# Performance work log

Measured on AMD Instinct MI355X. Metric: run time of the kernel, lower is better.

## Reference

```python
import jax, jax.numpy as jnp
import numpy as np

D = 1e-6
B, N, E, K = 128, 512, 512, 256


def _lower_median_abs(x, axis):
    # torch.median returns the LOWER of the two middle values for even counts
    n = x.shape[axis]
    s = jnp.sort(jnp.abs(x), axis=axis)
    return jnp.take(s, (n - 1) // 2, axis=axis)


def _bounds_from_cauchy(head, errors, k):
    # errors: (B, E, *head.shape[1:]); E divisible by k in this config
    b, e = errors.shape[0], errors.shape[1]
    tail = errors.shape[2:]
    chunks = errors.reshape(b, e // k, k, *tail)
    l1 = _lower_median_abs(chunks, axis=2).sum(axis=1)
    return head - l1, head + l1


def _relaxed_exp(h, errs, noise, lb, ub):
    is_tight = ub == lb
    lam_s = (jnp.exp(ub) - jnp.exp(lb)) / (ub - lb + D)
    lam = jnp.minimum(lam_s, jnp.exp(lb + 1.0 - 0.1))
    ub0 = jnp.where(lam > lam_s, jnp.exp(lb) - lam * lb, jnp.exp(ub) - lam * ub)
    mu = 0.5 * (lam * (1.0 - jnp.log(lam)) + ub0)
    delta = 0.5 * (ub0 - lam * (1.0 - jnp.log(lam)))
    lam = jnp.where(is_tight, 0.0, lam)
    mu = jnp.where(is_tight, jnp.exp(ub), mu)
    delta = jnp.where(is_tight, 0.0, delta)
    new_head = h * lam + mu
    new_errs = jnp.concatenate([errs * lam[:, None], delta[:, None] * noise], axis=1)
    return new_head, new_errs


def _relaxed_log(h, errs, noise, lb, ub):
    is_tight = ub == lb
    lam_s = (jnp.log(ub) - jnp.log(lb + D)) / (ub - lb + D)
    lam = lam_s
    lb0 = jnp.where(lam < lam_s, jnp.log(ub) - ub * lam, jnp.log(lb + D) - lb * lam)
    mu = 0.5 * (-jnp.log(lam) - 1.0 + lb0)
    delta = 0.5 * (-jnp.log(lam) - 1.0 - lb0)
    lam = jnp.where(is_tight, 0.0, lam)
    mu = jnp.where(is_tight, jnp.log(ub), mu)
    delta = jnp.where(is_tight, 0.0, delta)
    new_head = h * lam + mu
    new_errs = jnp.concatenate([errs * lam[:, None], delta[:, None] * noise], axis=1)
    return new_head, new_errs


def setup_inputs() -> dict:
    key = jax.random.key(0)
    k1, k2, k3, k4 = jax.random.split(key, 4)
    curr_head = jax.random.normal(k1, (B, N), dtype=jnp.float32)
    # small error magnitudes keep exp/log relaxation bounds valid (lb of log stage > 0)
    curr_errors = 1e-3 * jax.random.normal(k2, (B * E, N), dtype=jnp.float32)
    cauchy_exp = jax.random.cauchy(k3, (B, K, N), dtype=jnp.float32)
    cauchy_log = jax.random.cauchy(k4, (B, K), dtype=jnp.float32)
    return {"curr_head": curr_head, "curr_errors": curr_errors,
            "cauchy_exp": cauchy_exp, "cauchy_log": cauchy_log, "k": K}


def reference(curr_head, curr_errors, cauchy_exp, cauchy_log, k):
    b, n = curr_head.shape
    max_head = jax.lax.stop_gradient(jnp.max(curr_head, axis=1, keepdims=True))  # (B,1)
    temp_head = curr_head - max_head                         # (B,N)
    errs = curr_errors.reshape(b, -1, n)                     # (B,E,N)
    lb, ub = _bounds_from_cauchy(temp_head, errs, k)
    exp_head, exp_errs = _relaxed_exp(temp_head, errs, cauchy_exp, lb, ub)  # (B,N),(B,E+K,N)
    exp_head = exp_head.sum(axis=1)                          # (B,)
    exp_errs = exp_errs.sum(axis=2)                          # (B,E+K)
    lb2, ub2 = _bounds_from_cauchy(exp_head, exp_errs, k)
    ls_head, ls_errs = _relaxed_log(exp_head, exp_errs, cauchy_log, lb2, ub2)  # (B,),(B,E+2K)
    ls_head = ls_head + max_head[:, 0]
    return ls_head, ls_errs.reshape(-1)
```

## Files before the change

### kernel.cpp

```cpp
#include <hip/hip_runtime.h>
#include <cstdint>
#include <cstddef>

#define BB 128
#define NN 512
#define EE 512
#define KK 256
#define STR 17

__device__ __forceinline__ float wave_reduce_max(float v) {
#pragma unroll
  for (int off = 32; off >= 1; off >>= 1) v = fmaxf(v, __shfl_xor(v, off, 64));
  return v;
}
__device__ __forceinline__ float wave_reduce_sum(float v) {
#pragma unroll
  for (int off = 32; off >= 1; off >>= 1) v += __shfl_xor(v, off, 64);
  return v;
}

template <int CTRL>
__device__ __forceinline__ float dppz(float x) {
  return __int_as_float(__builtin_amdgcn_update_dpp(0, __float_as_int(x), CTRL, 0xf, 0xf, false));
}
template <int CTRL>
__device__ __forceinline__ float dppi(float x) {
  return __int_as_float(__builtin_amdgcn_update_dpp(__float_as_int(x), __float_as_int(x), CTRL, 0xf, 0xf, false));
}
__device__ __forceinline__ float wave_sum64(float x) {
  x += dppz<0x111>(x); x += dppz<0x112>(x); x += dppz<0x114>(x); x += dppz<0x118>(x);
  x += dppz<0x142>(x); x += dppz<0x143>(x);
  return __int_as_float(__builtin_amdgcn_readlane(__float_as_int(x), 63));
}
__device__ __forceinline__ float wave_max64nn(float x) {
  x = fmaxf(x, dppz<0x111>(x)); x = fmaxf(x, dppz<0x112>(x));
  x = fmaxf(x, dppz<0x114>(x)); x = fmaxf(x, dppz<0x118>(x));
  x = fmaxf(x, dppz<0x142>(x)); x = fmaxf(x, dppz<0x143>(x));
  return __int_as_float(__builtin_amdgcn_readlane(__float_as_int(x), 63));
}
__device__ __forceinline__ float wave_min64(float x) {
  x = fminf(x, dppi<0x111>(x)); x = fminf(x, dppi<0x112>(x));
  x = fminf(x, dppi<0x114>(x)); x = fminf(x, dppi<0x118>(x));
  x = fminf(x, dppi<0x142>(x)); x = fminf(x, dppi<0x143>(x));
  return __int_as_float(__builtin_amdgcn_readlane(__float_as_int(x), 63));
}

__device__ __forceinline__ float wave_median256_fast(float a0, float a1, float a2, float a3) {
  float S = wave_sum64((a0 + a1) + (a2 + a3));
  float mean = S * 0.00390625f;
  float lo = 0.f, hi = S * 1.0000002f + 1e-37f;
  int c_lo = 0, c_hi = 256;
  float piv = 0.845f * mean;
  float ans = 0.f;
  bool have = false;
#pragma unroll 1
  for (int it = 0; it < 34; ++it) {
    if (!(piv > lo && piv < hi)) piv = 0.5f * (lo + hi);
    int cnt = __popcll(__ballot(a0 < piv)) + __popcll(__ballot(a1 < piv)) +
              __popcll(__ballot(a2 < piv)) + __popcll(__ballot(a3 < piv));
    if (cnt == 128) {
      float m = fmaxf(fmaxf(a0 < piv ? a0 : 0.f, a1 < piv ? a1 : 0.f),
                      fmaxf(a2 < piv ? a2 : 0.f, a3 < piv ? a3 : 0.f));
      ans = wave_max64nn(m); have = true; break;
    }
    if (cnt == 127) {
      float m = fminf(fminf(a0 >= piv ? a0 : 3.4e38f, a1 >= piv ? a1 : 3.4e38f),
                      fminf(a2 >= piv ? a2 : 3.4e38f, a3 >= piv ? a3 : 3.4e38f));
      ans = wave_min64(m); have = true; break;
    }
    if (cnt < 127) { lo = piv; c_lo = cnt; } else { hi = piv; c_hi = cnt; }
    if (it == 0) piv = piv + (127.5f - (float)cnt) * mean * 0.0077f;
    else piv = lo + (hi - lo) * ((127.5f - (float)c_lo) / (float)(c_hi - c_lo));
    if (it >= 10) piv = 0.5f * (lo + hi);
  }
  if (!have) {
    float m = fmaxf(fmaxf(a0 < hi ? a0 : 0.f, a1 < hi ? a1 : 0.f),
                    fmaxf(a2 < hi ? a2 : 0.f, a3 < hi ? a3 : 0.f));
    ans = wave_max64nn(m);
  }
  return ans;
}

__global__ __launch_bounds__(1024, 8) void kfused(
    const float* __restrict__ head, const float* __restrict__ errs,
    float* __restrict__ ws_delta, float* __restrict__ ws_htpart,
    float* __restrict__ ws_epart) {
  __shared__ float tile[512 * STR];
  __shared__ float medbuf[32];
  __shared__ float lambuf[16];
  __shared__ float redm[16];
  const int blk = blockIdx.x;
  const int b = blk >> 5, g = blk & 31;
  const int n0 = g * 16;
  const int tid = threadIdx.x, wave = tid >> 6, lane = tid & 63;

  float m = (tid < NN) ? head[(size_t)b * NN + tid] : -3.4e38f;
  m = wave_reduce_max(m);
  if (lane == 0) redm[wave] = m;

  const int tr = tid >> 2, tc = (tid & 3) * 4;
  const float* src = errs + (size_t)b * EE * NN + n0 + tc;
#pragma unroll
  for (int i = 0; i < 2; ++i) {
    int row = i * 256 + tr;
    float4 v = *(const float4*)(src + (size_t)row * NN);
    float* dst = &tile[row * STR + tc];
    dst[0] = v.x; dst[1] = v.y; dst[2] = v.z; dst[3] = v.w;
  }
  __syncthreads();

#pragma unroll 1
  for (int j = 0; j < 2; ++j) {
    int p = wave * 2 + j;
    int col = p & 15;
    int rb = (p >> 4) * 256;
    float a0 = fabsf(tile[(rb + lane) * STR + col]);
    float a1 = fabsf(tile[(rb + lane + 64) * STR + col]);
    float a2 = fabsf(tile[(rb + lane + 128) * STR + col]);
    float a3 = fabsf(tile[(rb + lane + 192) * STR + col]);
    float med = wave_median256_fast(a0, a1, a2, a3);
    if (lane == 0) medbuf[p] = med;
  }
  __syncthreads();

  float htp = 0.f;
  if (tid < 16) {
    float hmax = fmaxf(
        fmaxf(fmaxf(fmaxf(redm[0], redm[1]), fmaxf(redm[2], redm[3])),
              fmaxf(fmaxf(redm[4], redm[5]), fmaxf(redm[6], redm[7]))),
        fmaxf(fmaxf(fmaxf(redm[8], redm[9]), fmaxf(redm[10], redm[11])),
              fmaxf(fmaxf(redm[12], redm[13]), fmaxf(redm[14], redm[15]))));
    int n = n0 + tid;
    float l1 = medbuf[tid] + medbuf[16 + tid];
    float th = head[(size_t)b * NN + n] - hmax;
    float lb = th - l1, ub = th + l1;
    float lam, mu, delta;
    if (ub == lb) {
      lam = 0.f; mu = expf(ub); delta = 0.f;
    } else {
      float elb = expf(lb), eub = expf(ub);
      float lam_s = (eub - elb) / (ub - lb + 1e-6f);
      lam = fminf(lam_s, expf(lb + 0.9f));
      float ub0 = (lam > lam_s) ? (elb - lam * lb) : (eub - lam * ub);
      float t = lam * (1.f - logf(lam));
      mu = 0.5f * (t + ub0);
      delta = 0.5f * (ub0 - t);
    }
    lambuf[tid] = lam;
    ws_delta[(size_t)b * NN + n] = delta;
    htp = th * lam + mu;
  }
  if (wave == 0) {
    float s = wave_reduce_sum(htp);
    if (lane == 0) ws_htpart[b * 32 + g] = s;
  }
  __syncthreads();

  if (tid < NN) {
    float s0 = 0.f;
#pragma unroll
    for (int j = 0; j < 16; ++j) s0 = fmaf(tile[tid * STR + j], lambuf[j], s0);
    ws_epart[((size_t)(b * 32 + g)) * 512 + tid] = s0;
  }
}

__global__ __launch_bounds__(256) void kcexp(
    const float* __restrict__ cexp, const float* __restrict__ ws_delta,
    float* __restrict__ ws_ee2) {
  const int blk = blockIdx.x;
  const int b = blk >> 4, seg = blk & 15;
  const int wave = threadIdx.x >> 6, lane = threadIdx.x & 63;
  const float* wsrc = ws_delta + (size_t)b * NN;
  float4 wa = *(const float4*)(wsrc + 4 * lane);
  float4 wb = *(const float4*)(wsrc + 256 + 4 * lane);
  const int r0 = seg * 16 + wave * 4;
  const float* base = cexp + (size_t)b * KK * NN;
  float* out = ws_ee2 + (size_t)b * KK;
  float s0, s1, s2, s3;
  {
    const float* rp = base + (size_t)r0 * NN;
    float4 x = *(const float4*)(rp + 4 * lane);
    float4 y = *(const float4*)(rp + 256 + 4 * lane);
    s0 = x.x * wa.x + x.y * wa.y + x.z * wa.z + x.w * wa.w +
         y.x * wb.x + y.y * wb.y + y.z * wb.z + y.w * wb.w;
  }
  {
    const float* rp = base + (size_t)(r0 + 1) * NN;
    float4 x = *(const float4*)(rp + 4 * lane);
    float4 y = *(const float4*)(rp + 256 + 4 * lane);
    s1 = x.x * wa.x + x.y * wa.y + x.z * wa.z + x.w * wa.w +
         y.x * wb.x + y.y * wb.y + y.z * wb.z + y.w * wb.w;
  }
  {
    const float* rp = base + (size_t)(r0 + 2) * NN;
    float4 x = *(const float4*)(rp + 4 * lane);
    float4 y = *(const float4*)(rp + 256 + 4 * lane);
    s2 = x.x * wa.x + x.y * wa.y + x.z * wa.z + x.w * wa.w +
         y.x * wb.x + y.y * wb.y + y.z * wb.z + y.w * wb.w;
  }
  {
    const float* rp = base + (size_t)(r0 + 3) * NN;
    float4 x = *(const float4*)(rp + 4 * lane);
    float4 y = *(const float4*)(rp + 256 + 4 * lane);
    s3 = x.x * wa.x + x.y * wa.y + x.z * wa.z + x.w * wa.w +
         y.x * wb.x + y.y * wb.y + y.z * wb.z + y.w * wb.w;
  }
  s0 = wave_sum64(s0);
  s1 = wave_sum64(s1);
  s2 = wave_sum64(s2);
  s3 = wave_sum64(s3);
  if (lane == 0) {
    out[r0] = s0; out[r0 + 1] = s1; out[r0 + 2] = s2; out[r0 + 3] = s3;
  }
}

__global__ __launch_bounds__(256) void kstage3(
    const float* __restrict__ head, const float* __restrict__ clog,
    const float* __restrict__ ws_htpart, const float* __restrict__ ws_epart,
    const float* __restrict__ ws_ee2, float* __restrict__ out) {
  __shared__ float eb[768];
  __shared__ float redm[4];
  __shared__ float meds[3];
  __shared__ float sc[2];
  __shared__ float ehsh;
  const int b = blockIdx.x;
  const int tid = threadIdx.x, wave = tid >> 6, lane = tid & 63;

  float m = fmaxf(head[(size_t)b * NN + tid], head[(size_t)b * NN + 256 + tid]);
  m = wave_reduce_max(m);
  if (lane == 0) redm[wave] = m;

  float acc0 = 0.f, acc1 = 0.f;
  const float* pp = ws_epart + (size_t)b * 32 * 512;
#pragma unroll
  for (int g = 0; g < 32; ++g) {
    acc0 += pp[g * 512 + tid];
    acc1 += pp[g * 512 + 256 + tid];
  }
  eb[tid] = acc0;
  eb[tid + 256] = acc1;
  eb[tid + 512] = ws_ee2[(size_t)b * KK + tid];
  __syncthreads();

  if (wave < 3) {
    const float* p = eb + wave * 256;
    float a0 = fabsf(p[lane]), a1 = fabsf(p[lane + 64]);
    float a2 = fabsf(p[lane + 128]), a3 = fabsf(p[lane + 192]);
    float med = wave_median256_fast(a0, a1, a2, a3);
    if (lane == 0) meds[wave] = med;
  } else {
    float v = (lane < 32) ? ws_htpart[b * 32 + lane] : 0.f;
    v = wave_reduce_sum(v);
    if (lane == 0) ehsh = v;
  }
  __syncthreads();

  if (tid == 0) {
    float hmax = fmaxf(fmaxf(redm[0], redm[1]), fmaxf(redm[2], redm[3]));
    float eh = ehsh;
    float l1 = meds[0] + meds[1] + meds[2];
    float lb = eh - l1, ub = eh + l1;
    float lam, mu, delta;
    if (ub == lb) {
      lam = 0.f; mu = logf(ub); delta = 0.f;
    } else {
      float llb = logf(lb + 1e-6f);
      float lam_s = (logf(ub) - llb) / (ub - lb + 1e-6f);
      lam = lam_s;
      float lb0 = llb - lb * lam;
      float t = -logf(lam) - 1.f;
      mu = 0.5f * (t + lb0);
      delta = 0.5f * (t - lb0);
    }
    sc[0] = lam; sc[1] = delta;
    out[b] = eh * lam + mu + hmax;
  }
  __syncthreads();
  float lam = sc[0], delta = sc[1];
  float* ob = out + BB + (size_t)b * 1024;
  ob[tid] = eb[tid] * lam;
  ob[tid + 256] = eb[tid + 256] * lam;
  ob[tid + 512] = eb[tid + 512] * lam;
  ob[tid + 768] = delta * clog[(size_t)b * KK + tid];
}

extern "C" void kernel_launch(void* const* d_in, const int* in_sizes, int n_in,
                              void* d_out, int out_size, void* d_ws, size_t ws_size,
                              hipStream_t stream) {
  const float* head = (const float*)d_in[0];
  const float* errs = (const float*)d_in[1];
  const float* cexp = (const float*)d_in[2];
  const float* clog = (const float*)d_in[3];
  float* out = (float*)d_out;

  float* ws = (float*)d_ws;
  float* ws_delta = ws;
  float* ws_htpart = ws_delta + BB * NN;
  float* ws_ee2 = ws_htpart + BB * 32;
  float* ws_epart = ws_ee2 + BB * KK;

  hipLaunchKernelGGL(kfused, dim3(BB * 32), dim3(1024), 0, stream,
                     head, errs, ws_delta, ws_htpart, ws_epart);
  hipLaunchKernelGGL(kcexp, dim3(BB * 16), dim3(256), 0, stream,
                     cexp, ws_delta, ws_ee2);
  hipLaunchKernelGGL(kstage3, dim3(BB), dim3(256), 0, stream,
                     head, clog, ws_htpart, ws_epart, ws_ee2, out);
}
```

Measured before the change: 275.5 us.

## Halve fused block size and interleave four median searches per wave

The fused kernel now runs with 512 threads per block instead of 1024, so each wave handles four column-half medians instead of two. The four pivot-based median selections are interleaved in one loop so their ballot/popcount rounds can overlap and hide latency across independent searches. The tile load and the final error-partial loop drop their tid<NN guards, and the head-max reduction uses 8 waves. The cost is more registers per thread for the four sets of state, plus lower occupancy hints.

```diff
diff --git a/kernel.cpp b/kernel.cpp
--- a/kernel.cpp
+++ b/kernel.cpp
@@ -81,55 +81,101 @@
   return ans;
 }
 
-__global__ __launch_bounds__(1024, 8) void kfused(
+__global__ __launch_bounds__(512, 2) void kfused(
     const float* __restrict__ head, const float* __restrict__ errs,
     float* __restrict__ ws_delta, float* __restrict__ ws_htpart,
     float* __restrict__ ws_epart) {
   __shared__ float tile[512 * STR];
   __shared__ float medbuf[32];
   __shared__ float lambuf[16];
-  __shared__ float redm[16];
+  __shared__ float redm[8];
   const int blk = blockIdx.x;
   const int b = blk >> 5, g = blk & 31;
   const int n0 = g * 16;
   const int tid = threadIdx.x, wave = tid >> 6, lane = tid & 63;
 
-  float m = (tid < NN) ? head[(size_t)b * NN + tid] : -3.4e38f;
+  float m = head[(size_t)b * NN + tid];
   m = wave_reduce_max(m);
   if (lane == 0) redm[wave] = m;
 
   const int tr = tid >> 2, tc = (tid & 3) * 4;
   const float* src = errs + (size_t)b * EE * NN + n0 + tc;
 #pragma unroll
-  for (int i = 0; i < 2; ++i) {
-    int row = i * 256 + tr;
+  for (int i = 0; i < 4; ++i) {
+    int row = i * 128 + tr;
     float4 v = *(const float4*)(src + (size_t)row * NN);
     float* dst = &tile[row * STR + tc];
     dst[0] = v.x; dst[1] = v.y; dst[2] = v.z; dst[3] = v.w;
   }
   __syncthreads();
 
-#pragma unroll 1
-  for (int j = 0; j < 2; ++j) {
-    int p = wave * 2 + j;
+  float A[4][4];
+  float lo4[4], hi4[4], piv4[4], ans4[4], mean4[4];
+  int clo4[4], chi4[4];
+  bool done4[4];
+#pragma unroll
+  for (int j = 0; j < 4; ++j) {
+    int p = wave * 4 + j;
     int col = p & 15;
     int rb = (p >> 4) * 256;
-    float a0 = fabsf(tile[(rb + lane) * STR + col]);
-    float a1 = fabsf(tile[(rb + lane + 64) * STR + col]);
-    float a2 = fabsf(tile[(rb + lane + 128) * STR + col]);
-    float a3 = fabsf(tile[(rb + lane + 192) * STR + col]);
-    float med = wave_median256_fast(a0, a1, a2, a3);
-    if (lane == 0) medbuf[p] = med;
+    A[j][0] = fabsf(tile[(rb + lane) * STR + col]);
+    A[j][1] = fabsf(tile[(rb + lane + 64) * STR + col]);
+    A[j][2] = fabsf(tile[(rb + lane + 128) * STR + col]);
+    A[j][3] = fabsf(tile[(rb + lane + 192) * STR + col]);
+  }
+#pragma unroll
+  for (int j = 0; j < 4; ++j) {
+    float S = wave_sum64((A[j][0] + A[j][1]) + (A[j][2] + A[j][3]));
+    mean4[j] = S * 0.00390625f;
+    lo4[j] = 0.f; clo4[j] = 0;
+    hi4[j] = S * 1.0000002f + 1e-37f; chi4[j] = 256;
+    piv4[j] = 0.845f * mean4[j];
+    ans4[j] = 0.f; done4[j] = false;
+  }
+#pragma unroll 1
+  for (int it = 0; it < 34; ++it) {
+    if (done4[0] && done4[1] && done4[2] && done4[3]) break;
+#pragma unroll
+    for (int j = 0; j < 4; ++j) {
+      if (done4[j]) continue;
+      float piv = piv4[j];
+      if (!(piv > lo4[j] && piv < hi4[j])) piv = 0.5f * (lo4[j] + hi4[j]);
+      int cnt = __popcll(__ballot(A[j][0] < piv)) + __popcll(__ballot(A[j][1] < piv)) +
+                __popcll(__ballot(A[j][2] < piv)) + __popcll(__ballot(A[j][3] < piv));
+      if (cnt == 128) {
+        float mm = fmaxf(fmaxf(A[j][0] < piv ? A[j][0] : 0.f, A[j][1] < piv ? A[j][1] : 0.f),
+                         fmaxf(A[j][2] < piv ? A[j][2] : 0.f, A[j][3] < piv ? A[j][3] : 0.f));
+        ans4[j] = wave_max64nn(mm); done4[j] = true;
+      } else if (cnt == 127) {
+        float mm = fminf(fminf(A[j][0] >= piv ? A[j][0] : 3.4e38f, A[j][1] >= piv ? A[j][1] : 3.4e38f),
+                         fminf(A[j][2] >= piv ? A[j][2] : 3.4e38f, A[j][3] >= piv ? A[j][3] : 3.4e38f));
+        ans4[j] = wave_min64(mm); done4[j] = true;
+      } else {
+        if (cnt < 127) { lo4[j] = piv; clo4[j] = cnt; } else { hi4[j] = piv; chi4[j] = cnt; }
+        float np;
+        if (it == 0) np = piv + (127.5f - (float)cnt) * mean4[j] * 0.0077f;
+        else np = lo4[j] + (hi4[j] - lo4[j]) *
+                      ((127.5f - (float)clo4[j]) / (float)(chi4[j] - clo4[j]));
+        if (it >= 10) np = 0.5f * (lo4[j] + hi4[j]);
+        piv4[j] = np;
+      }
+    }
+  }
+#pragma unroll
+  for (int j = 0; j < 4; ++j) {
+    if (!done4[j]) {
+      float mm = fmaxf(fmaxf(A[j][0] < hi4[j] ? A[j][0] : 0.f, A[j][1] < hi4[j] ? A[j][1] : 0.f),
+                       fmaxf(A[j][2] < hi4[j] ? A[j][2] : 0.f, A[j][3] < hi4[j] ? A[j][3] : 0.f));
+      ans4[j] = wave_max64nn(mm);
+    }
+    if (lane == 0) medbuf[wave * 4 + j] = ans4[j];
   }
   __syncthreads();
 
   float htp = 0.f;
   if (tid < 16) {
-    float hmax = fmaxf(
-        fmaxf(fmaxf(fmaxf(redm[0], redm[1]), fmaxf(redm[2], redm[3])),
-              fmaxf(fmaxf(redm[4], redm[5]), fmaxf(redm[6], redm[7]))),
-        fmaxf(fmaxf(fmaxf(redm[8], redm[9]), fmaxf(redm[10], redm[11])),
-              fmaxf(fmaxf(redm[12], redm[13]), fmaxf(redm[14], redm[15]))));
+    float hmax = fmaxf(fmaxf(fmaxf(redm[0], redm[1]), fmaxf(redm[2], redm[3])),
+                       fmaxf(fmaxf(redm[4], redm[5]), fmaxf(redm[6], redm[7])));
     int n = n0 + tid;
     float l1 = medbuf[tid] + medbuf[16 + tid];
     float th = head[(size_t)b * NN + n] - hmax;
@@ -156,12 +202,10 @@
   }
   __syncthreads();
 
-  if (tid < NN) {
-    float s0 = 0.f;
-#pragma unroll
-    for (int j = 0; j < 16; ++j) s0 = fmaf(tile[tid * STR + j], lambuf[j], s0);
-    ws_epart[((size_t)(b * 32 + g)) * 512 + tid] = s0;
-  }
+  float s0 = 0.f;
+#pragma unroll
+  for (int j = 0; j < 16; ++j) s0 = fmaf(tile[tid * STR + j], lambuf[j], s0);
+  ws_epart[((size_t)(b * 32 + g)) * 512 + tid] = s0;
 }
 
 __global__ __launch_bounds__(256) void kcexp(
@@ -299,7 +343,7 @@
   float* ws_ee2 = ws_htpart + BB * 32;
   float* ws_epart = ws_ee2 + BB * KK;
 
-  hipLaunchKernelGGL(kfused, dim3(BB * 32), dim3(1024), 0, stream,
+  hipLaunchKernelGGL(kfused, dim3(BB * 32), dim3(512), 0, stream,
                      head, errs, ws_delta, ws_htpart, ws_epart);
   hipLaunchKernelGGL(kcexp, dim3(BB * 16), dim3(256), 0, stream,
                      cexp, ws_delta, ws_ee2);
```

After: 266.7 us. -3.2%, faster.
